# Kernel tuning notes

Measured on AMD Instinct MI355X. Metric: run time of the kernel, lower is better.

The kernel has to match this reference:

```python
import jax, jax.numpy as jnp
import numpy as np


def setup_inputs() -> dict:
    key = jax.random.key(0)
    ks = jax.random.split(key, 5)
    B, S, D, U = 4, 2048, 1024, 1024
    scale = 1.0 / np.sqrt(D)
    return {
        "query": jax.random.normal(ks[0], (B, S, D), dtype=jnp.float32),
        "value": jax.random.normal(ks[1], (B, S, D), dtype=jnp.float32),
        "Wq": jax.random.normal(ks[2], (D, U), dtype=jnp.float32) * scale,
        "bq": jnp.zeros((U,), dtype=jnp.float32),
        "Wk": jax.random.normal(ks[3], (D, U), dtype=jnp.float32) * scale,
        "bk": jnp.zeros((U,), dtype=jnp.float32),
        "Wv": jax.random.normal(ks[4], (D, U), dtype=jnp.float32) * scale,
        "bv": jnp.zeros((U,), dtype=jnp.float32),
    }


def reference(query, value, Wq, bq, Wk, bk, Wv, bv):
    # Dense projections (last-dim matmul + bias)
    Q = jnp.einsum("bsd,du->bsu", query, Wq) + bq   # [B,Sq,U]
    K = jnp.einsum("btd,du->btu", value, Wk) + bk   # [B,Sk,U]
    V = jnp.einsum("btd,du->btu", value, Wv) + bv   # [B,Sk,U]
    d_k = jnp.asarray(K.shape[-1], dtype=jnp.float32)
    scores = jnp.einsum("bsu,btu->bst", Q, K) / jnp.sqrt(d_k)  # [B,Sq,Sk]
    weights = jax.nn.softmax(scores, axis=-1)
    return jnp.einsum("bst,btu->bsu", weights, V)   # [B,Sq,U]
```

## Files before the change

kernel.cpp:

```cpp
#include <hip/hip_runtime.h>
#include <hip/hip_bf16.h>
#include <stdint.h>

#define DEVINL __device__ __forceinline__

typedef __attribute__((ext_vector_type(4))) float f32x4;
typedef __attribute__((ext_vector_type(8))) __bf16 bfv8;
typedef __attribute__((ext_vector_type(8))) short s16x8;
typedef __attribute__((ext_vector_type(4))) short s16x4;

DEVINL short f2bf(float f) {
  union { float f; unsigned u; } v; v.f = f;
  unsigned r = v.u + 0x7FFFu + ((v.u >> 16) & 1u);
  return (short)(r >> 16);
}
DEVINL float bf2f(short h) {
  union { unsigned u; float f; } v; v.u = ((unsigned)(unsigned short)h) << 16;
  return v.f;
}
DEVINL void gload_lds16(const void* g, void* l) {
  __builtin_amdgcn_global_load_lds((__attribute__((address_space(1))) unsigned*)(g),
                                   (__attribute__((address_space(3))) unsigned*)(l),
                                   16, 0, 0);
}
#define S_BARRIER() __builtin_amdgcn_s_barrier()
#define LGKM0() asm volatile("s_waitcnt lgkmcnt(0)" ::: "memory")
#define MEMORD() asm volatile("" ::: "memory")
DEVINL void vmwait(int n) {
  if (n >= 8) asm volatile("s_waitcnt vmcnt(8)" ::: "memory");
  else if (n >= 4) asm volatile("s_waitcnt vmcnt(4)" ::: "memory");
  else asm volatile("s_waitcnt vmcnt(0)" ::: "memory");
}

DEVINL void gemm32_core(const short* __restrict__ Ag, const short* __restrict__ Bg,
                        int lda, int ldb, int m0, int n0, int nkt,
                        short* lds, f32x4 (&acc)[8][4]) {
  const int tid = threadIdx.x;
  const int w = tid >> 6, l = tid & 63;
  const int wm = w >> 2, wn = w & 3;
  const int lr = l & 15, lg = l >> 4;
  const int stg_row = w * 16 + (l >> 2);
  const int stg_col = (((l & 3) ^ ((l >> 3) & 3)) << 3);
  const int ck = ((lg ^ ((lr >> 1) & 3)) << 3);
  const int aro = (wm * 128 + lr) * 32 + ck;
  const int bro = (wn * 64 + lr) * 32 + ck;
  const int dU0 = (w * 16) * 32, dU1 = (128 + w * 16) * 32;

#pragma unroll
  for (int t = 0; t < 3; ++t) {
    short* Ab = lds + t * 16384;
    short* Bb = Ab + 8192;
    gload_lds16(Ag + (size_t)(m0 + stg_row) * lda + t * 32 + stg_col, Ab + dU0);
    gload_lds16(Ag + (size_t)(m0 + 128 + stg_row) * lda + t * 32 + stg_col, Ab + dU1);
    gload_lds16(Bg + (size_t)(n0 + stg_row) * ldb + t * 32 + stg_col, Bb + dU0);
    gload_lds16(Bg + (size_t)(n0 + 128 + stg_row) * ldb + t * 32 + stg_col, Bb + dU1);
  }
  vmwait(8); S_BARRIER(); MEMORD();

  bfv8 a[4], b[4];
#pragma unroll 1
  for (int kt = 0; kt < nkt; ++kt) {
    const short* Ab = lds + (kt & 3) * 16384;
    const short* Bb = Ab + 8192;
    const int ks = kt + 3;
    short* sA = lds + (ks & 3) * 16384;
    short* sB = sA + 8192;
#pragma unroll
    for (int mf = 0; mf < 4; ++mf) a[mf] = *(const bfv8*)(Ab + aro + mf * 512);
#pragma unroll
    for (int nf = 0; nf < 4; ++nf) b[nf] = *(const bfv8*)(Bb + bro + nf * 512);
    if (ks < nkt) {
      gload_lds16(Ag + (size_t)(m0 + stg_row) * lda + ks * 32 + stg_col, sA + dU0);
      gload_lds16(Ag + (size_t)(m0 + 128 + stg_row) * lda + ks * 32 + stg_col, sA + dU1);
    }
    S_BARRIER(); LGKM0();
    __builtin_amdgcn_s_setprio(1);
#pragma unroll
    for (int mf = 0; mf < 4; ++mf)
#pragma unroll
      for (int nf = 0; nf < 4; ++nf)
        acc[mf][nf] = __builtin_amdgcn_mfma_f32_16x16x32_bf16(a[mf], b[nf], acc[mf][nf], 0, 0, 0);
    __builtin_amdgcn_s_setprio(0);
    S_BARRIER(); MEMORD();
#pragma unroll
    for (int mf = 0; mf < 4; ++mf) a[mf] = *(const bfv8*)(Ab + aro + 2048 + mf * 512);
    if (ks < nkt) {
      gload_lds16(Bg + (size_t)(n0 + stg_row) * ldb + ks * 32 + stg_col, sB + dU0);
      gload_lds16(Bg + (size_t)(n0 + 128 + stg_row) * ldb + ks * 32 + stg_col, sB + dU1);
    }
    if (kt + 1 < nkt) vmwait(ks < nkt ? 8 : (kt + 2 < nkt ? 4 : 0));
    S_BARRIER(); LGKM0();
    __builtin_amdgcn_s_setprio(1);
#pragma unroll
    for (int mf = 0; mf < 4; ++mf)
#pragma unroll
      for (int nf = 0; nf < 4; ++nf)
        acc[4 + mf][nf] = __builtin_amdgcn_mfma_f32_16x16x32_bf16(a[mf], b[nf], acc[4 + mf][nf], 0, 0, 0);
    __builtin_amdgcn_s_setprio(0);
    S_BARRIER(); MEMORD();
  }
}

__global__ __launch_bounds__(256) void cast_kernel(const float* __restrict__ q,
                                                   const float* __restrict__ v,
                                                   short* __restrict__ Qc, short* __restrict__ Vc) {
  const float* src = blockIdx.y ? v : q;
  short* dst = blockIdx.y ? Vc : Qc;
  const size_t i = ((size_t)blockIdx.x * 256 + threadIdx.x) * 8;
  f32x4 x0 = *(const f32x4*)(src + i);
  f32x4 x1 = *(const f32x4*)(src + i + 4);
  s16x8 o;
#pragma unroll
  for (int j = 0; j < 4; ++j) { o[j] = f2bf(x0[j]); o[4 + j] = f2bf(x1[j]); }
  *(s16x8*)(dst + i) = o;
}

__global__ __launch_bounds__(256) void wt_kernel(
    const float* __restrict__ Wq, const float* __restrict__ Wk, const float* __restrict__ Wv,
    short* __restrict__ WTq, short* __restrict__ WTk, short* __restrict__ WTv) {
  __shared__ float tile[64][65];
  const float* W = (blockIdx.z == 0) ? Wq : (blockIdx.z == 1) ? Wk : Wv;
  short* WT = (blockIdx.z == 0) ? WTq : (blockIdx.z == 1) ? WTk : WTv;
  const int k0 = (blockIdx.x & 15) << 6;
  const int n0 = (blockIdx.x >> 4) << 6;
  const int c = threadIdx.x & 63, r0 = threadIdx.x >> 6;
#pragma unroll
  for (int i = 0; i < 16; ++i) {
    int r = (i << 2) + r0;
    tile[r][c] = W[(size_t)(k0 + r) * 1024 + n0 + c];
  }
  __syncthreads();
#pragma unroll
  for (int i = 0; i < 16; ++i) {
    int a = (i << 2) + r0;
    WT[(size_t)(n0 + a) * 1024 + k0 + c] = f2bf(tile[c][a]);
  }
}

__global__ __launch_bounds__(512, 2) void proj8_kernel(
    const short* __restrict__ Qc, const short* __restrict__ Vc,
    const short* __restrict__ WTq, const short* __restrict__ WTk, const short* __restrict__ WTv,
    const float* __restrict__ bq, const float* __restrict__ bk, const float* __restrict__ bv,
    short* __restrict__ Qb, short* __restrict__ Kb, short* __restrict__ VT) {
  __shared__ short lds[65536];
  const int bm = blockIdx.x & 31, bn = blockIdx.x >> 5;
  const int sel = bn >> 2;
  const short* A = (sel == 0) ? Qc : Vc;
  const short* BT = (sel == 0) ? WTq : (sel == 1) ? WTk : WTv;
  const float* bias = (sel == 0) ? bq : (sel == 1) ? bk : bv;
  const int m0 = bm * 256, n0 = (bn & 3) * 256;
  f32x4 acc[8][4];
#pragma unroll
  for (int i = 0; i < 8; ++i)
#pragma unroll
    for (int j = 0; j < 4; ++j) acc[i][j] = (f32x4){0.f, 0.f, 0.f, 0.f};
  gemm32_core(A, BT, 1024, 1024, m0, n0, 32, lds, acc);
  const int tid = threadIdx.x;
  const int w = tid >> 6, l = tid & 63;
  const int wm = w >> 2, wn = w & 3, lr = l & 15, lg = l >> 4;
#pragma unroll
  for (int i = 0; i < 8; ++i) {
    const int row0 = m0 + wm * 128 + (i >> 2) * 64 + (i & 3) * 16 + lg * 4;
#pragma unroll
    for (int nf = 0; nf < 4; ++nf) {
      const int col = n0 + wn * 64 + nf * 16 + lr;
      const float bb = bias[col];
      if (sel < 2) {
        short* O = sel ? Kb : Qb;
#pragma unroll
        for (int j = 0; j < 4; ++j)
          O[(size_t)(row0 + j) * 1024 + col] = f2bf(acc[i][nf][j] + bb);
      } else {
        const int bidx = row0 >> 11, t = row0 & 2047;
        s16x4 pk;
#pragma unroll
        for (int j = 0; j < 4; ++j) pk[j] = f2bf(acc[i][nf][j] + bb);
        *(s16x4*)(VT + ((size_t)bidx * 1024 + col) * 2048 + t) = pk;
      }
    }
  }
}

__global__ __launch_bounds__(512, 2) void qkt8_kernel(const short* __restrict__ Qb,
                                                      const short* __restrict__ Kb,
                                                      short* __restrict__ Sb) {
  __shared__ short lds[65536];
  const int bt = blockIdx.y;
  const int bm = blockIdx.x >> 3, bn = blockIdx.x & 7;
  const short* A = Qb + (size_t)bt * 2097152;
  const short* B = Kb + (size_t)bt * 2097152;
  short* O = Sb + (size_t)bt * 4194304;
  const int m0 = bm * 256, n0 = bn * 256;
  f32x4 acc[8][4];
#pragma unroll
  for (int i = 0; i < 8; ++i)
#pragma unroll
    for (int j = 0; j < 4; ++j) acc[i][j] = (f32x4){0.f, 0.f, 0.f, 0.f};
  gemm32_core(A, B, 1024, 1024, m0, n0, 32, lds, acc);
  const int tid = threadIdx.x;
  const int w = tid >> 6, l = tid & 63;
  const int wm = w >> 2, wn = w & 3, lr = l & 15, lg = l >> 4;
#pragma unroll
  for (int i = 0; i < 8; ++i) {
    const int row0 = m0 + wm * 128 + (i >> 2) * 64 + (i & 3) * 16 + lg * 4;
#pragma unroll
    for (int nf = 0; nf < 4; ++nf) {
      const int col = n0 + wn * 64 + nf * 16 + lr;
#pragma unroll
      for (int j = 0; j < 4; ++j)
        O[(size_t)(row0 + j) * 2048 + col] = f2bf(acc[i][nf][j] * 0.03125f);
    }
  }
}

__global__ __launch_bounds__(512, 2) void pv8_kernel(const short* __restrict__ Sb,
                                                     const short* __restrict__ VT,
                                                     float* __restrict__ Out) {
  __shared__ short lds[65536];
  const int bt = blockIdx.y;
  const int bm = blockIdx.x >> 2, bn = blockIdx.x & 3;
  const short* A = Sb + (size_t)bt * 4194304;
  const short* B = VT + (size_t)bt * 2097152;
  float* O = Out + (size_t)bt * 2097152;
  const int m0 = bm * 256, n0 = bn * 256;
  f32x4 acc[8][4];
#pragma unroll
  for (int i = 0; i < 8; ++i)
#pragma unroll
    for (int j = 0; j < 4; ++j) acc[i][j] = (f32x4){0.f, 0.f, 0.f, 0.f};
  gemm32_core(A, B, 2048, 2048, m0, n0, 64, lds, acc);
  const int tid = threadIdx.x;
  const int w = tid >> 6, l = tid & 63;
  const int wm = w >> 2, wn = w & 3, lr = l & 15, lg = l >> 4;
#pragma unroll
  for (int i = 0; i < 8; ++i) {
    const int row0 = m0 + wm * 128 + (i >> 2) * 64 + (i & 3) * 16 + lg * 4;
#pragma unroll
    for (int nf = 0; nf < 4; ++nf) {
      const int col = n0 + wn * 64 + nf * 16 + lr;
#pragma unroll
      for (int j = 0; j < 4; ++j)
        O[(size_t)(row0 + j) * 1024 + col] = acc[i][nf][j];
    }
  }
}

__global__ __launch_bounds__(256) void softmax_kernel(short* __restrict__ Sb) {
  const size_t row = blockIdx.x;
  short* p = Sb + row * 2048;
  const int tid = threadIdx.x;
  const int w = tid >> 6, l = tid & 63;
  s16x8 v = *(const s16x8*)(p + tid * 8);
  float f[8];
#pragma unroll
  for (int j = 0; j < 8; ++j) f[j] = bf2f(v[j]);
  float m = f[0];
#pragma unroll
  for (int j = 1; j < 8; ++j) m = fmaxf(m, f[j]);
#pragma unroll
  for (int o = 32; o > 0; o >>= 1) m = fmaxf(m, __shfl_xor(m, o, 64));
  __shared__ float redm[4], reds[4];
  if (l == 0) redm[w] = m;
  __syncthreads();
  m = fmaxf(fmaxf(redm[0], redm[1]), fmaxf(redm[2], redm[3]));
  float s = 0.f;
#pragma unroll
  for (int j = 0; j < 8; ++j) { f[j] = __expf(f[j] - m); s += f[j]; }
#pragma unroll
  for (int o = 32; o > 0; o >>= 1) s += __shfl_xor(s, o, 64);
  if (l == 0) reds[w] = s;
  __syncthreads();
  s = reds[0] + reds[1] + reds[2] + reds[3];
  const float inv = 1.f / s;
  s16x8 o8;
#pragma unroll
  for (int j = 0; j < 8; ++j) o8[j] = f2bf(f[j] * inv);
  *(s16x8*)(p + tid * 8) = o8;
}

extern "C" void kernel_launch(void* const* d_in, const int* in_sizes, int n_in,
                              void* d_out, int out_size, void* d_ws, size_t ws_size,
                              hipStream_t stream) {
  const float* query = (const float*)d_in[0];
  const float* value = (const float*)d_in[1];
  const float* Wq = (const float*)d_in[2];
  const float* bq = (const float*)d_in[3];
  const float* Wk = (const float*)d_in[4];
  const float* bk = (const float*)d_in[5];
  const float* Wv = (const float*)d_in[6];
  const float* bv = (const float*)d_in[7];

  char* ws = (char*)d_ws;
  short* WTq = (short*)(ws);
  short* WTk = (short*)(ws + ((size_t)2 << 20));
  short* WTv = (short*)(ws + ((size_t)4 << 20));
  short* Qc  = (short*)(ws + ((size_t)6 << 20));
  short* Vc  = (short*)(ws + ((size_t)22 << 20));
  short* Sb  = (short*)(ws + ((size_t)6 << 20));
  short* Qb  = (short*)(ws + ((size_t)38 << 20));
  short* Kb  = (short*)(ws + ((size_t)54 << 20));
  short* VT  = (short*)(ws + ((size_t)70 << 20));

  cast_kernel<<<dim3(4096, 2), 256, 0, stream>>>(query, value, Qc, Vc);
  wt_kernel<<<dim3(256, 1, 3), 256, 0, stream>>>(Wq, Wk, Wv, WTq, WTk, WTv);

  proj8_kernel<<<dim3(384), 512, 0, stream>>>(Qc, Vc, WTq, WTk, WTv, bq, bk, bv, Qb, Kb, VT);

  qkt8_kernel<<<dim3(64, 4), 512, 0, stream>>>(Qb, Kb, Sb);

  softmax_kernel<<<dim3(8192), 256, 0, stream>>>(Sb);

  pv8_kernel<<<dim3(32, 4), 512, 0, stream>>>(Sb, VT, (float*)d_out);
}
```

Before: 212.7 us.

## Split V projection into narrow-tile kernel with LDS-staged transpose, merge prep kernels

Templates the GEMM core on the B-tile width so the V projection can use 256x128 tiles and run as its own 256-block launch, with the Q/K projections in another 256-block launch. The V output is transposed through LDS and written as 16-byte coalesced stores instead of scattered 8-byte stores. The cast and weight-transpose kernels are merged into one launch. The aim is to balance wave counts across the GPU and fix poorly coalesced VT writes. The cost is one extra projection launch and a narrower tile for V, which gives less reuse per block.

```diff
diff --git a/kernel.cpp b/kernel.cpp
--- a/kernel.cpp
+++ b/kernel.cpp
@@ -26,15 +26,16 @@
 #define S_BARRIER() __builtin_amdgcn_s_barrier()
 #define LGKM0() asm volatile("s_waitcnt lgkmcnt(0)" ::: "memory")
 #define MEMORD() asm volatile("" ::: "memory")
-DEVINL void vmwait(int n) {
-  if (n >= 8) asm volatile("s_waitcnt vmcnt(8)" ::: "memory");
-  else if (n >= 4) asm volatile("s_waitcnt vmcnt(4)" ::: "memory");
-  else asm volatile("s_waitcnt vmcnt(0)" ::: "memory");
-}
-
-DEVINL void gemm32_core(const short* __restrict__ Ag, const short* __restrict__ Bg,
-                        int lda, int ldb, int m0, int n0, int nkt,
-                        short* lds, f32x4 (&acc)[8][4]) {
+template <int N> DEVINL void vmwaitc() {
+  asm volatile("s_waitcnt vmcnt(%0)" :: "i"(N) : "memory");
+}
+
+template <int BU, int NF>
+DEVINL void gemm_core(const short* __restrict__ Ag, const short* __restrict__ Bg,
+                      int lda, int ldb, int m0, int n0, int nkt,
+                      short* lds, f32x4 (&acc)[8][NF]) {
+  constexpr int U = 2 + BU;
+  constexpr int SLOT = 8192 + BU * 4096;
   const int tid = threadIdx.x;
   const int w = tid >> 6, l = tid & 63;
   const int wm = w >> 2, wn = w & 3;
@@ -43,118 +44,125 @@
   const int stg_col = (((l & 3) ^ ((l >> 3) & 3)) << 3);
   const int ck = ((lg ^ ((lr >> 1) & 3)) << 3);
   const int aro = (wm * 128 + lr) * 32 + ck;
-  const int bro = (wn * 64 + lr) * 32 + ck;
-  const int dU0 = (w * 16) * 32, dU1 = (128 + w * 16) * 32;
+  const int bro = 8192 + (wn * (NF * 16) + lr) * 32 + ck;
+  const int dW = w * 512;
 
 #pragma unroll
   for (int t = 0; t < 3; ++t) {
-    short* Ab = lds + t * 16384;
-    short* Bb = Ab + 8192;
-    gload_lds16(Ag + (size_t)(m0 + stg_row) * lda + t * 32 + stg_col, Ab + dU0);
-    gload_lds16(Ag + (size_t)(m0 + 128 + stg_row) * lda + t * 32 + stg_col, Ab + dU1);
-    gload_lds16(Bg + (size_t)(n0 + stg_row) * ldb + t * 32 + stg_col, Bb + dU0);
-    gload_lds16(Bg + (size_t)(n0 + 128 + stg_row) * ldb + t * 32 + stg_col, Bb + dU1);
-  }
-  vmwait(8); S_BARRIER(); MEMORD();
-
-  bfv8 a[4], b[4];
+    short* S = lds + t * SLOT;
+    gload_lds16(Ag + (size_t)(m0 + stg_row) * lda + t * 32 + stg_col, S + dW);
+    gload_lds16(Ag + (size_t)(m0 + 128 + stg_row) * lda + t * 32 + stg_col, S + 4096 + dW);
+#pragma unroll
+    for (int u = 0; u < BU; ++u)
+      gload_lds16(Bg + (size_t)(n0 + u * 128 + stg_row) * ldb + t * 32 + stg_col,
+                  S + 8192 + u * 4096 + dW);
+  }
+  vmwaitc<2 * U>(); S_BARRIER(); MEMORD();
+
+  bfv8 a[4], b[NF];
 #pragma unroll 1
   for (int kt = 0; kt < nkt; ++kt) {
-    const short* Ab = lds + (kt & 3) * 16384;
-    const short* Bb = Ab + 8192;
+    const short* Sc = lds + (kt & 3) * SLOT;
     const int ks = kt + 3;
-    short* sA = lds + (ks & 3) * 16384;
-    short* sB = sA + 8192;
-#pragma unroll
-    for (int mf = 0; mf < 4; ++mf) a[mf] = *(const bfv8*)(Ab + aro + mf * 512);
-#pragma unroll
-    for (int nf = 0; nf < 4; ++nf) b[nf] = *(const bfv8*)(Bb + bro + nf * 512);
+    short* Ss = lds + (ks & 3) * SLOT;
+#pragma unroll
+    for (int mf = 0; mf < 4; ++mf) a[mf] = *(const bfv8*)(Sc + aro + mf * 512);
+#pragma unroll
+    for (int nf = 0; nf < NF; ++nf) b[nf] = *(const bfv8*)(Sc + bro + nf * 512);
     if (ks < nkt) {
-      gload_lds16(Ag + (size_t)(m0 + stg_row) * lda + ks * 32 + stg_col, sA + dU0);
-      gload_lds16(Ag + (size_t)(m0 + 128 + stg_row) * lda + ks * 32 + stg_col, sA + dU1);
+      gload_lds16(Ag + (size_t)(m0 + stg_row) * lda + ks * 32 + stg_col, Ss + dW);
+      gload_lds16(Ag + (size_t)(m0 + 128 + stg_row) * lda + ks * 32 + stg_col, Ss + 4096 + dW);
     }
     S_BARRIER(); LGKM0();
     __builtin_amdgcn_s_setprio(1);
 #pragma unroll
     for (int mf = 0; mf < 4; ++mf)
 #pragma unroll
-      for (int nf = 0; nf < 4; ++nf)
+      for (int nf = 0; nf < NF; ++nf)
         acc[mf][nf] = __builtin_amdgcn_mfma_f32_16x16x32_bf16(a[mf], b[nf], acc[mf][nf], 0, 0, 0);
     __builtin_amdgcn_s_setprio(0);
     S_BARRIER(); MEMORD();
 #pragma unroll
-    for (int mf = 0; mf < 4; ++mf) a[mf] = *(const bfv8*)(Ab + aro + 2048 + mf * 512);
+    for (int mf = 0; mf < 4; ++mf) a[mf] = *(const bfv8*)(Sc + aro + 2048 + mf * 512);
     if (ks < nkt) {
-      gload_lds16(Bg + (size_t)(n0 + stg_row) * ldb + ks * 32 + stg_col, sB + dU0);
-      gload_lds16(Bg + (size_t)(n0 + 128 + stg_row) * ldb + ks * 32 + stg_col, sB + dU1);
-    }
-    if (kt + 1 < nkt) vmwait(ks < nkt ? 8 : (kt + 2 < nkt ? 4 : 0));
+#pragma unroll
+      for (int u = 0; u < BU; ++u)
+        gload_lds16(Bg + (size_t)(n0 + u * 128 + stg_row) * ldb + ks * 32 + stg_col,
+                    Ss + 8192 + u * 4096 + dW);
+    }
+    if (kt + 1 < nkt) {
+      if (ks < nkt) vmwaitc<2 * U>();
+      else if (kt + 2 < nkt) vmwaitc<U>();
+      else vmwaitc<0>();
+    }
     S_BARRIER(); LGKM0();
     __builtin_amdgcn_s_setprio(1);
 #pragma unroll
     for (int mf = 0; mf < 4; ++mf)
 #pragma unroll
-      for (int nf = 0; nf < 4; ++nf)
+      for (int nf = 0; nf < NF; ++nf)
         acc[4 + mf][nf] = __builtin_amdgcn_mfma_f32_16x16x32_bf16(a[mf], b[nf], acc[4 + mf][nf], 0, 0, 0);
     __builtin_amdgcn_s_setprio(0);
     S_BARRIER(); MEMORD();
   }
 }
 
-__global__ __launch_bounds__(256) void cast_kernel(const float* __restrict__ q,
-                                                   const float* __restrict__ v,
-                                                   short* __restrict__ Qc, short* __restrict__ Vc) {
-  const float* src = blockIdx.y ? v : q;
-  short* dst = blockIdx.y ? Vc : Qc;
-  const size_t i = ((size_t)blockIdx.x * 256 + threadIdx.x) * 8;
-  f32x4 x0 = *(const f32x4*)(src + i);
-  f32x4 x1 = *(const f32x4*)(src + i + 4);
-  s16x8 o;
-#pragma unroll
-  for (int j = 0; j < 4; ++j) { o[j] = f2bf(x0[j]); o[4 + j] = f2bf(x1[j]); }
-  *(s16x8*)(dst + i) = o;
-}
-
-__global__ __launch_bounds__(256) void wt_kernel(
+__global__ __launch_bounds__(256) void prep_kernel(
+    const float* __restrict__ q, const float* __restrict__ v,
     const float* __restrict__ Wq, const float* __restrict__ Wk, const float* __restrict__ Wv,
+    short* __restrict__ Qc, short* __restrict__ Vc,
     short* __restrict__ WTq, short* __restrict__ WTk, short* __restrict__ WTv) {
   __shared__ float tile[64][65];
-  const float* W = (blockIdx.z == 0) ? Wq : (blockIdx.z == 1) ? Wk : Wv;
-  short* WT = (blockIdx.z == 0) ? WTq : (blockIdx.z == 1) ? WTk : WTv;
-  const int k0 = (blockIdx.x & 15) << 6;
-  const int n0 = (blockIdx.x >> 4) << 6;
-  const int c = threadIdx.x & 63, r0 = threadIdx.x >> 6;
-#pragma unroll
-  for (int i = 0; i < 16; ++i) {
-    int r = (i << 2) + r0;
-    tile[r][c] = W[(size_t)(k0 + r) * 1024 + n0 + c];
-  }
-  __syncthreads();
-#pragma unroll
-  for (int i = 0; i < 16; ++i) {
-    int a = (i << 2) + r0;
-    WT[(size_t)(n0 + a) * 1024 + k0 + c] = f2bf(tile[c][a]);
-  }
-}
-
-__global__ __launch_bounds__(512, 2) void proj8_kernel(
+  const int bx = blockIdx.x;
+  if (bx < 8192) {
+    const float* src = (bx < 4096) ? q : v;
+    short* dst = (bx < 4096) ? Qc : Vc;
+    const size_t i = ((size_t)(bx & 4095) * 256 + threadIdx.x) * 8;
+    f32x4 x0 = *(const f32x4*)(src + i);
+    f32x4 x1 = *(const f32x4*)(src + i + 4);
+    s16x8 o;
+#pragma unroll
+    for (int j = 0; j < 4; ++j) { o[j] = f2bf(x0[j]); o[4 + j] = f2bf(x1[j]); }
+    *(s16x8*)(dst + i) = o;
+  } else {
+    const int z = (bx - 8192) >> 8, xx = (bx - 8192) & 255;
+    const float* W = (z == 0) ? Wq : (z == 1) ? Wk : Wv;
+    short* WT = (z == 0) ? WTq : (z == 1) ? WTk : WTv;
+    const int k0 = (xx & 15) << 6, n0 = (xx >> 4) << 6;
+    const int c = threadIdx.x & 63, r0 = threadIdx.x >> 6;
+#pragma unroll
+    for (int i = 0; i < 16; ++i) {
+      int r = (i << 2) + r0;
+      tile[r][c] = W[(size_t)(k0 + r) * 1024 + n0 + c];
+    }
+    __syncthreads();
+#pragma unroll
+    for (int i = 0; i < 16; ++i) {
+      int a = (i << 2) + r0;
+      WT[(size_t)(n0 + a) * 1024 + k0 + c] = f2bf(tile[c][a]);
+    }
+  }
+}
+
+__global__ __launch_bounds__(512, 2) void qkproj_kernel(
     const short* __restrict__ Qc, const short* __restrict__ Vc,
-    const short* __restrict__ WTq, const short* __restrict__ WTk, const short* __restrict__ WTv,
-    const float* __restrict__ bq, const float* __restrict__ bk, const float* __restrict__ bv,
-    short* __restrict__ Qb, short* __restrict__ Kb, short* __restrict__ VT) {
+    const short* __restrict__ WTq, const short* __restrict__ WTk,
+    const float* __restrict__ bq, const float* __restrict__ bk,
+    short* __restrict__ Qb, short* __restrict__ Kb) {
   __shared__ short lds[65536];
-  const int bm = blockIdx.x & 31, bn = blockIdx.x >> 5;
+  const int bm = blockIdx.x >> 3, bn = blockIdx.x & 7;
   const int sel = bn >> 2;
-  const short* A = (sel == 0) ? Qc : Vc;
-  const short* BT = (sel == 0) ? WTq : (sel == 1) ? WTk : WTv;
-  const float* bias = (sel == 0) ? bq : (sel == 1) ? bk : bv;
+  const short* A = sel ? Vc : Qc;
+  const short* BT = sel ? WTk : WTq;
+  const float* bias = sel ? bk : bq;
+  short* O = sel ? Kb : Qb;
   const int m0 = bm * 256, n0 = (bn & 3) * 256;
   f32x4 acc[8][4];
 #pragma unroll
   for (int i = 0; i < 8; ++i)
 #pragma unroll
     for (int j = 0; j < 4; ++j) acc[i][j] = (f32x4){0.f, 0.f, 0.f, 0.f};
-  gemm32_core(A, BT, 1024, 1024, m0, n0, 32, lds, acc);
+  gemm_core<2, 4>(A, BT, 1024, 1024, m0, n0, 32, lds, acc);
   const int tid = threadIdx.x;
   const int w = tid >> 6, l = tid & 63;
   const int wm = w >> 2, wn = w & 3, lr = l & 15, lg = l >> 4;
@@ -165,19 +173,49 @@
     for (int nf = 0; nf < 4; ++nf) {
       const int col = n0 + wn * 64 + nf * 16 + lr;
       const float bb = bias[col];
-      if (sel < 2) {
-        short* O = sel ? Kb : Qb;
-#pragma unroll
-        for (int j = 0; j < 4; ++j)
-          O[(size_t)(row0 + j) * 1024 + col] = f2bf(acc[i][nf][j] + bb);
-      } else {
-        const int bidx = row0 >> 11, t = row0 & 2047;
-        s16x4 pk;
-#pragma unroll
-        for (int j = 0; j < 4; ++j) pk[j] = f2bf(acc[i][nf][j] + bb);
-        *(s16x4*)(VT + ((size_t)bidx * 1024 + col) * 2048 + t) = pk;
-      }
-    }
+#pragma unroll
+      for (int j = 0; j < 4; ++j)
+        O[(size_t)(row0 + j) * 1024 + col] = f2bf(acc[i][nf][j] + bb);
+    }
+  }
+}
+
+__global__ __launch_bounds__(512, 2) void vproj_kernel(
+    const short* __restrict__ Vc, const short* __restrict__ WTv,
+    const float* __restrict__ bv, short* __restrict__ VT) {
+  __shared__ short lds[49152];
+  const int bm = blockIdx.x >> 3, bn = blockIdx.x & 7;
+  const int m0 = bm * 256, n0 = bn * 128;
+  f32x4 acc[8][2];
+#pragma unroll
+  for (int i = 0; i < 8; ++i)
+#pragma unroll
+    for (int j = 0; j < 2; ++j) acc[i][j] = (f32x4){0.f, 0.f, 0.f, 0.f};
+  gemm_core<1, 2>(Vc, WTv, 1024, 1024, m0, n0, 32, lds, acc);
+  const int tid = threadIdx.x;
+  const int w = tid >> 6, l = tid & 63;
+  const int wm = w >> 2, wn = w & 3, lr = l & 15, lg = l >> 4;
+  __syncthreads();
+#pragma unroll
+  for (int i = 0; i < 8; ++i) {
+    const int tl = wm * 128 + (i >> 2) * 64 + (i & 3) * 16 + lg * 4;
+#pragma unroll
+    for (int nf = 0; nf < 2; ++nf) {
+      const int ul = wn * 32 + nf * 16 + lr;
+      const float bb = bv[n0 + ul];
+#pragma unroll
+      for (int j = 0; j < 4; ++j)
+        lds[ul * 264 + tl + j] = f2bf(acc[i][nf][j] + bb);
+    }
+  }
+  __syncthreads();
+  const int b = m0 >> 11, t0 = m0 & 2047;
+#pragma unroll
+  for (int it = 0; it < 8; ++it) {
+    const int cid = it * 512 + tid;
+    const int u = cid >> 5, tc = cid & 31;
+    s16x8 v8 = *(const s16x8*)&lds[u * 264 + tc * 8];
+    *(s16x8*)(VT + ((size_t)b * 1024 + n0 + u) * 2048 + t0 + tc * 8) = v8;
   }
 }
 
@@ -196,7 +234,7 @@
   for (int i = 0; i < 8; ++i)
 #pragma unroll
     for (int j = 0; j < 4; ++j) acc[i][j] = (f32x4){0.f, 0.f, 0.f, 0.f};
-  gemm32_core(A, B, 1024, 1024, m0, n0, 32, lds, acc);
+  gemm_core<2, 4>(A, B, 1024, 1024, m0, n0, 32, lds, acc);
   const int tid = threadIdx.x;
   const int w = tid >> 6, l = tid & 63;
   const int wm = w >> 2, wn = w & 3, lr = l & 15, lg = l >> 4;
@@ -228,7 +266,7 @@
   for (int i = 0; i < 8; ++i)
 #pragma unroll
     for (int j = 0; j < 4; ++j) acc[i][j] = (f32x4){0.f, 0.f, 0.f, 0.f};
-  gemm32_core(A, B, 2048, 2048, m0, n0, 64, lds, acc);
+  gemm_core<2, 4>(A, B, 2048, 2048, m0, n0, 64, lds, acc);
   const int tid = threadIdx.x;
   const int w = tid >> 6, l = tid & 63;
   const int wm = w >> 2, wn = w & 3, lr = l & 15, lg = l >> 4;
@@ -301,10 +339,10 @@
   short* Kb  = (short*)(ws + ((size_t)54 << 20));
   short* VT  = (short*)(ws + ((size_t)70 << 20));
 
-  cast_kernel<<<dim3(4096, 2), 256, 0, stream>>>(query, value, Qc, Vc);
-  wt_kernel<<<dim3(256, 1, 3), 256, 0, stream>>>(Wq, Wk, Wv, WTq, WTk, WTv);
-
-  proj8_kernel<<<dim3(384), 512, 0, stream>>>(Qc, Vc, WTq, WTk, WTv, bq, bk, bv, Qb, Kb, VT);
+  prep_kernel<<<dim3(8960), 256, 0, stream>>>(query, value, Wq, Wk, Wv, Qc, Vc, WTq, WTk, WTv);
+
+  qkproj_kernel<<<dim3(256), 512, 0, stream>>>(Qc, Vc, WTq, WTk, bq, bk, Qb, Kb);
+  vproj_kernel<<<dim3(256), 512, 0, stream>>>(Vc, WTv, bv, VT);
 
   qkt8_kernel<<<dim3(64, 4), 512, 0, stream>>>(Qb, Kb, Sb);
 
```

Result: no change. 208.6 us (-1.9%).
